# Kernel tuning notes

Measured on AMD Instinct MI355X. Metric: run time of the kernel, lower is better.

The kernel has to match this reference:

```python
import jax, jax.numpy as jnp
import numpy as np

# CUBA-LIF constants (from LavaNetwork.__init__ with beta=0.95)
THRESHOLD = 1.0
CURRENT_DECAY = 1.0   # current[t] = (1-1.0)*current[t-1] + input[t] == input[t]
VOLTAGE_DECAY = 1.0 - 0.95  # = 0.05, so v[t] = 0.95*v[t-1] + cur[t]

N_INPUT, N_HIDDEN, N_OUTPUT = 512, 2048, 4 * 64
B, T = 32, 1024


def setup_inputs() -> dict:
    key = jax.random.key(0)
    kx, k1, k2, k3, k4 = jax.random.split(key, 5)
    x = (jax.random.uniform(kx, (B, N_INPUT, T)) < 0.1).astype(jnp.float32)
    # learned params (Linear with bias); small scale so spiking is reasonable
    w1 = jax.random.normal(k1, (N_HIDDEN, N_INPUT), dtype=jnp.float32) * (1.0 / np.sqrt(N_INPUT))
    b1 = jax.random.normal(k2, (N_HIDDEN,), dtype=jnp.float32) * 0.01
    w2 = jax.random.normal(k3, (N_OUTPUT, N_HIDDEN), dtype=jnp.float32) * (1.0 / np.sqrt(N_HIDDEN))
    b2 = jax.random.normal(k4, (N_OUTPUT,), dtype=jnp.float32) * 0.01
    return {"x": x, "w1": w1, "b1": b1, "w2": w2, "b2": b2}


def _cuba_lif(cur):
    """CUBA neuron with current_decay=1 (current==synaptic input),
    leaky-integrate voltage, fire at threshold, reset voltage to 0.
    cur: (B, N, T) -> spikes (B, N, T)."""
    beta_v = 1.0 - VOLTAGE_DECAY  # 0.95

    def step(v, c_t):
        v = v * beta_v + c_t
        s = (v >= THRESHOLD).astype(v.dtype)
        v = v * (1.0 - s)  # reset-to-zero on spike (Loihi behavior)
        return v, s

    cur_t = jnp.moveaxis(cur, -1, 0)  # (T, B, N)
    v0 = jnp.zeros(cur.shape[:-1], cur.dtype)
    _, spk = jax.lax.scan(step, v0, cur_t)
    return jnp.moveaxis(spk, 0, -1)  # (B, N, T)


def reference(x, w1, b1, w2, b2):
    # layer 1: synapse (einsum 'bit,oi->bot' + bias) -> CUBA neuron
    cur1 = jnp.einsum('bit,oi->bot', x, w1) + b1[None, :, None]
    spk1 = _cuba_lif(cur1)
    # layer 2
    cur2 = jnp.einsum('bit,oi->bot', spk1, w2) + b2[None, :, None]
    spk2 = _cuba_lif(cur2)
    return (spk1, spk2)
```

## Files before the change

### kernel.cpp

```cpp
#include <hip/hip_runtime.h>


typedef int i32x4 __attribute__((ext_vector_type(4)));
typedef _Float16 f16x8 __attribute__((ext_vector_type(8)));
typedef _Float16 f16x4 __attribute__((ext_vector_type(4)));
typedef float f32x4 __attribute__((ext_vector_type(4)));

#define GLDS(g, l) __builtin_amdgcn_global_load_lds( \
    (const __attribute__((address_space(1))) void*)(g), \
    (__attribute__((address_space(3))) void*)(l), 16, 0, 0)

#define INV231 4.656612873077392578125e-10


__global__ __launch_bounds__(256) void prep_w8(const float* __restrict__ A,
                                               signed char* __restrict__ wp,
                                               int M, int K)
{
    long gt = (long)blockIdx.x * 256 + threadIdx.x;
    int kq4 = K >> 2;
    int m = (int)(gt / kq4), kq = (int)(gt % kq4);
    int k0 = kq * 4;
    int kt = k0 >> 6, kin = k0 & 63;
    int cw = ((kin >> 4) ^ (m >> 1)) & 3;
    float4 w = *(const float4*)&A[(long)m * K + k0];
    float wv[4] = {w.x, w.y, w.z, w.w};
    int pack[4] = {0, 0, 0, 0};
#pragma unroll
    for (int e = 0; e < 4; e++) {
        long k64 = (long)rint((double)wv[e] * 2147483648.0);
#pragma unroll
        for (int j = 0; j < 3; j++) {
            long r = ((k64 + 128) & 255) - 128;
            pack[j] |= ((int)r & 255) << (e * 8);
            k64 = (k64 - r) >> 8;
        }
        pack[3] |= ((int)k64 & 255) << (e * 8);
    }
#pragma unroll
    for (int p = 0; p < 4; p++)
        *(int*)&wp[(((long)kt * 4 + p) * M + m) * 64 + cw * 16 + (kin & 15)] = pack[p];
}

__global__ __launch_bounds__(256) void prep_x8(const float* __restrict__ x,
                                               unsigned char* __restrict__ xt)
{
    __shared__ float xs[64][68];
    const int b = blockIdx.z, i0 = blockIdx.y * 64, t0 = blockIdx.x * 64;
    const float* xb = x + ((long)b * 512 + i0) * 1024 + t0;
#pragma unroll
    for (int p = 0; p < 4; p++) {
        int f = threadIdx.x + p * 256;
        int i = f >> 4, t4 = (f & 15) * 4;
        *(float4*)&xs[i][t4] = *(const float4*)&xb[(long)i * 1024 + t4];
    }
    __syncthreads();
    int tt = threadIdx.x >> 2, c = threadIdx.x & 3;
    unsigned char bytes[16];
#pragma unroll
    for (int j = 0; j < 16; j++)
        bytes[j] = (unsigned char)xs[c * 16 + j][tt];
    *(uint4*)&xt[(((long)b * 8 + (i0 >> 6)) * 1024 + t0 + tt) * 64 + c * 16] =
        *(uint4*)bytes;
}

template <bool TRANS, int NITER, int CHUNK>
__global__ __launch_bounds__(256, 2) void gemm_i8(
    const signed char* __restrict__ wp,
    const unsigned char* __restrict__ act,
    const float* __restrict__ bias,
    float* __restrict__ C,
    int M)
{
    constexpr int NCHUNK = NITER / CHUNK;
    __shared__ signed char Ws[CHUNK][4][32][64];

    const int b = blockIdx.y;
    const int m0 = blockIdx.z * 32, t0 = blockIdx.x * 256;
    const int tid = threadIdx.x, lane = tid & 63, wave = tid >> 6;
    const int wt = t0 + wave * 64;
    const int lm = lane & 15, lq = lane >> 4;
    const int fro = ((lq ^ (lm >> 1)) & 3) * 16;
    const int gl_row = lane >> 2, gl_col = (lane & 3) * 16;

    const unsigned char* ab = act + (long)b * NITER * 1024 * 64;

    auto stage = [&](int cc) {
#pragma unroll
        for (int j = 0; j < CHUNK; ++j) {
            const int r = wave + 4 * j;
            const int kt = r >> 2, p = r & 3;
            const long kg = ((long)(cc * CHUNK + kt) * 4 + p);
            const signed char* g = wp + (kg * M + m0 + gl_row) * 64 + gl_col;
            GLDS(g, &Ws[kt][p][0][0]);
            GLDS(g + 16 * 64, &Ws[kt][p][16][0]);
        }
    };

    i32x4 acc[4][8];
#pragma unroll
    for (int p = 0; p < 4; p++)
#pragma unroll
        for (int q = 0; q < 8; q++) acc[p][q] = (i32x4)0;

    stage(0);
    i32x4 areg[2][4];
#pragma unroll
    for (int f = 0; f < 4; f++)
        areg[0][f] = *(const i32x4*)&ab[((long)(wt + f * 16 + lm)) * 64 + lq * 16];
    __syncthreads();

    for (int c = 0; c < NCHUNK; ++c) {
#pragma unroll
        for (int kk = 0; kk < CHUNK; ++kk) {
            {
                const int itv = c * CHUNK + kk;
                const long nx = (itv + 1 < NITER) ? itv + 1 : itv;
#pragma unroll
                for (int f = 0; f < 4; f++)
                    areg[(kk + 1) & 1][f] = *(const i32x4*)
                        &ab[(nx * 1024 + wt + f * 16 + lm) * 64 + lq * 16];
            }
#pragma unroll
            for (int p = 0; p < 4; p++) {
                i32x4 w0 = *(const i32x4*)&Ws[kk][p][lm][fro];
                i32x4 w1 = *(const i32x4*)&Ws[kk][p][16 + lm][fro];
                if (TRANS) {
#pragma unroll
                    for (int f = 0; f < 4; f++) {
                        acc[p][f * 2 + 0] = __builtin_amdgcn_mfma_i32_16x16x64_i8(
                            areg[kk & 1][f], w0, acc[p][f * 2 + 0], 0, 0, 0);
                        acc[p][f * 2 + 1] = __builtin_amdgcn_mfma_i32_16x16x64_i8(
                            areg[kk & 1][f], w1, acc[p][f * 2 + 1], 0, 0, 0);
                    }
                } else {
#pragma unroll
                    for (int f = 0; f < 4; f++) {
                        acc[p][0 + f] = __builtin_amdgcn_mfma_i32_16x16x64_i8(
                            w0, areg[kk & 1][f], acc[p][0 + f], 0, 0, 0);
                        acc[p][4 + f] = __builtin_amdgcn_mfma_i32_16x16x64_i8(
                            w1, areg[kk & 1][f], acc[p][4 + f], 0, 0, 0);
                    }
                }
            }
        }
        if (c + 1 < NCHUNK) {
            __syncthreads();
            stage(c + 1);
            __syncthreads();
        }
    }

    if (TRANS) {
        double bv[2];
        bv[0] = (double)bias[m0 + lm];
        bv[1] = (double)bias[m0 + 16 + lm];
        float* Cb = C + (long)b * 1024 * M;
#pragma unroll
        for (int tf = 0; tf < 4; tf++)
#pragma unroll
            for (int r = 0; r < 4; r++) {
                const int trow = wt + tf * 16 + lq * 4 + r;
#pragma unroll
                for (int mf = 0; mf < 2; mf++) {
                    long T = acc[3][tf * 2 + mf][r];
                    T = T * 256 + acc[2][tf * 2 + mf][r];
                    T = T * 256 + acc[1][tf * 2 + mf][r];
                    T = T * 256 + acc[0][tf * 2 + mf][r];
                    Cb[(long)trow * M + m0 + mf * 16 + lm] =
                        (float)((double)T * INV231 + bv[mf]);
                }
            }
    } else {
        float* Cb = C + (long)b * M * 1024;
#pragma unroll
        for (int mf = 0; mf < 2; mf++)
#pragma unroll
            for (int r = 0; r < 4; r++) {
                const int mrow = m0 + mf * 16 + lq * 4 + r;
                const double bv = (double)bias[mrow];
#pragma unroll
                for (int tf = 0; tf < 4; tf++) {
                    long T = acc[3][mf * 4 + tf][r];
                    T = T * 256 + acc[2][mf * 4 + tf][r];
                    T = T * 256 + acc[1][mf * 4 + tf][r];
                    T = T * 256 + acc[0][mf * 4 + tf][r];
                    Cb[(long)mrow * 1024 + wt + tf * 16 + lm] =
                        (float)((double)T * INV231 + bv);
                }
            }
    }
}


__global__ __launch_bounds__(256) void lif1_t(
    const float* __restrict__ ct,
    unsigned char* __restrict__ spk8,
    unsigned* __restrict__ mask_ws)
{
    const int b = blockIdx.y;
    const int m = blockIdx.x * 256 + threadIdx.x;
    const float* src = ct + (long)b * 1024 * 2048 + m;
    unsigned char* spb = spk8 + (((long)b * 32 + (m >> 6)) * 1024) * 64 + (m & 63);
    unsigned* mw = mask_ws + (long)b * 32 * 2048 + m;
    double v = 0.0;
    float c0[32], c1[32];
#pragma unroll
    for (int j = 0; j < 32; j++)
        c0[j] = src[(long)j * 2048];
    for (int tw = 0; tw < 32; tw += 2) {
#pragma unroll
        for (int j = 0; j < 32; j++)
            c1[j] = src[(long)((tw + 1) * 32 + j) * 2048];
        unsigned mword = 0;
#pragma unroll
        for (int j = 0; j < 32; j++) {
            v = 0.95 * v + (double)c0[j];
            bool s = v >= 1.0;
            mword |= (s ? 1u : 0u) << j;
            if (s) v = 0.0;
            spb[(long)(tw * 32 + j) * 64] = s ? 1 : 0;
        }
        mw[(long)tw * 2048] = mword;
        if (tw + 2 < 32) {
#pragma unroll
            for (int j = 0; j < 32; j++)
                c0[j] = src[(long)((tw + 2) * 32 + j) * 2048];
        }
        mword = 0;
#pragma unroll
        for (int j = 0; j < 32; j++) {
            v = 0.95 * v + (double)c1[j];
            bool s = v >= 1.0;
            mword |= (s ? 1u : 0u) << j;
            if (s) v = 0.0;
            spb[(long)((tw + 1) * 32 + j) * 64] = s ? 1 : 0;
        }
        mw[(long)(tw + 1) * 2048] = mword;
    }
}

__global__ __launch_bounds__(256) void expand_spk(
    const unsigned* __restrict__ mask_ws,
    float* __restrict__ spk1)
{
    __shared__ unsigned msk[8][32];
    const long rowbase = (long)blockIdx.x * 8;
    const int b = (int)(rowbase >> 11), m0 = (int)(rowbase & 2047);
    const int tid = threadIdx.x;
    {
        int w = tid >> 3, r = tid & 7;
        msk[r][w] = mask_ws[((long)b * 32 + w) * 2048 + m0 + r];
    }
    __syncthreads();
    const int r = tid >> 5, l5 = tid & 31;
    float* dst = spk1 + (rowbase + r) * 1024;
    const int sh = (l5 & 7) * 4;
#pragma unroll
    for (int j = 0; j < 8; j++) {
        const int t = l5 * 4 + j * 128;
        const unsigned w = msk[r][(l5 >> 3) + j * 4];
        float4 o;
        o.x = ((w >> sh) & 1u) ? 1.f : 0.f;
        o.y = ((w >> (sh + 1)) & 1u) ? 1.f : 0.f;
        o.z = ((w >> (sh + 2)) & 1u) ? 1.f : 0.f;
        o.w = ((w >> (sh + 3)) & 1u) ? 1.f : 0.f;
        *(float4*)&dst[t] = o;
    }
}

template <int RPB>
__global__ __launch_bounds__(256) void lif_lds(float* __restrict__ cur)
{
    __shared__ float cs[RPB][36];
    const long rowbase = (long)blockIdx.x * RPB;
    float* base = cur + rowbase * 1024;
    const int tid = threadIdx.x;
    double v = 0.0;
    const int NV = RPB * 32 / 4;
    for (int tc = 0; tc < 1024; tc += 32) {
        for (int f = tid; f < NV; f += 256) {
            int row = f >> 3, t4 = (f & 7) * 4;
            *(float4*)&cs[row][t4] = *(const float4*)&base[(long)row * 1024 + tc + t4];
        }
        __syncthreads();
        if (tid < RPB) {
#pragma unroll
            for (int j = 0; j < 32; j++) {
                v = 0.95 * v + (double)cs[tid][j];
                bool s = v >= 1.0;
                cs[tid][j] = s ? 1.f : 0.f;
                if (s) v = 0.0;
            }
        }
        __syncthreads();
        for (int f = tid; f < NV; f += 256) {
            int row = f >> 3, t4 = (f & 7) * 4;
            *(float4*)&base[(long)row * 1024 + tc + t4] = *(float4*)&cs[row][t4];
        }
        __syncthreads();
    }
}


__device__ inline void split3(float w, _Float16& q0, _Float16& q1, _Float16& q2) {
    float p0 = rintf(w * 4096.f) * 2.44140625e-4f;
    float r1 = w - p0;
    float p1s = rintf(r1 * 8388608.f) * 2.44140625e-4f;
    float r2 = r1 - p1s * 4.8828125e-4f;
    float p2s = rintf(r2 * 1.7179869184e10f) * 1.220703125e-4f;
    q0 = (_Float16)p0; q1 = (_Float16)p1s; q2 = (_Float16)p2s;
}

__global__ __launch_bounds__(256) void gemm_f16x3_kernel(
    const float* __restrict__ A, const float* __restrict__ Bmat,
    const float* __restrict__ bias, float* __restrict__ C,
    int M, int N, int K, long sB, long sC)
{
    __shared__ _Float16 As[3][128][40];
    __shared__ _Float16 Bsh[128][40];
    const int batch = blockIdx.z;
    const float* Bp = Bmat + (long)batch * sB;
    float* Cp = C + (long)batch * sC;
    const int m0 = blockIdx.y * 128, n0 = blockIdx.x * 128;
    const int tid = threadIdx.x, lane = tid & 63, wave = tid >> 6;
    const int wrow = (wave >> 1) * 64, wcol = (wave & 1) * 64;
    const int lm = lane & 15, lq = lane >> 4;
    const int a_mo = tid >> 3, a_kc = (tid & 7) * 4;
    const int b_kq = tid >> 5, b_nq = tid & 31;

    f32x4 acc[3][4][4];
#pragma unroll
    for (int p = 0; p < 3; p++)
#pragma unroll
        for (int i = 0; i < 4; i++)
#pragma unroll
            for (int j = 0; j < 4; j++) acc[p][i][j] = (f32x4)0.f;

    for (int k0 = 0; k0 < K; k0 += 32) {
#pragma unroll
        for (int i = 0; i < 4; i++) {
            const int m = i * 32 + a_mo;
            float4 w = *(const float4*)&A[(long)(m0 + m) * K + k0 + a_kc];
            _Float16 a0[4], a1[4], a2[4];
            split3(w.x, a0[0], a1[0], a2[0]);
            split3(w.y, a0[1], a1[1], a2[1]);
            split3(w.z, a0[2], a1[2], a2[2]);
            split3(w.w, a0[3], a1[3], a2[3]);
            *(f16x4*)&As[0][m][a_kc] = (f16x4){a0[0], a0[1], a0[2], a0[3]};
            *(f16x4*)&As[1][m][a_kc] = (f16x4){a1[0], a1[1], a1[2], a1[3]};
            *(f16x4*)&As[2][m][a_kc] = (f16x4){a2[0], a2[1], a2[2], a2[3]};
        }
        {
            float4 r0 = *(const float4*)&Bp[(long)(k0 + b_kq * 4 + 0) * N + n0 + b_nq * 4];
            float4 r1 = *(const float4*)&Bp[(long)(k0 + b_kq * 4 + 1) * N + n0 + b_nq * 4];
            float4 r2 = *(const float4*)&Bp[(long)(k0 + b_kq * 4 + 2) * N + n0 + b_nq * 4];
            float4 r3 = *(const float4*)&Bp[(long)(k0 + b_kq * 4 + 3) * N + n0 + b_nq * 4];
            *(f16x4*)&Bsh[b_nq * 4 + 0][b_kq * 4] =
                (f16x4){(_Float16)r0.x, (_Float16)r1.x, (_Float16)r2.x, (_Float16)r3.x};
            *(f16x4*)&Bsh[b_nq * 4 + 1][b_kq * 4] =
                (f16x4){(_Float16)r0.y, (_Float16)r1.y, (_Float16)r2.y, (_Float16)r3.y};
            *(f16x4*)&Bsh[b_nq * 4 + 2][b_kq * 4] =
                (f16x4){(_Float16)r0.z, (_Float16)r1.z, (_Float16)r2.z, (_Float16)r3.z};
            *(f16x4*)&Bsh[b_nq * 4 + 3][b_kq * 4] =
                (f16x4){(_Float16)r0.w, (_Float16)r1.w, (_Float16)r2.w, (_Float16)r3.w};
        }
        __syncthreads();
        f16x8 bf[4];
#pragma unroll
        for (int j = 0; j < 4; j++)
            bf[j] = *(const f16x8*)&Bsh[wcol + j * 16 + lm][lq * 8];
#pragma unroll
        for (int p = 0; p < 3; p++) {
            f16x8 af[4];
#pragma unroll
            for (int i = 0; i < 4; i++)
                af[i] = *(const f16x8*)&As[p][wrow + i * 16 + lm][lq * 8];
#pragma unroll
            for (int i = 0; i < 4; i++)
#pragma unroll
                for (int j = 0; j < 4; j++)
                    acc[p][i][j] = __builtin_amdgcn_mfma_f32_16x16x32_f16(
                        af[i], bf[j], acc[p][i][j], 0, 0, 0);
        }
        __syncthreads();
    }
#pragma unroll
    for (int i = 0; i < 4; i++)
#pragma unroll
        for (int r = 0; r < 4; r++) {
            const int row = m0 + wrow + i * 16 + lq * 4 + r;
            const double bv = (double)bias[row];
#pragma unroll
            for (int j = 0; j < 4; j++) {
                double s = (double)acc[0][i][j][r]
                         + (double)acc[1][i][j][r] * 4.8828125e-4
                         + (double)acc[2][i][j][r] * 4.76837158203125e-7 + bv;
                Cp[(long)row * N + n0 + wcol + j * 16 + lm] = (float)s;
            }
        }
}

__global__ __launch_bounds__(256) void lif_rows(float* __restrict__ data,
                                                long nrows, int T)
{
    long r = (long)blockIdx.x * blockDim.x + threadIdx.x;
    if (r >= nrows) return;
    float* p = data + r * (long)T;
    double v = 0.0;
    for (int t = 0; t < T; t += 4) {
        float4 c = *(float4*)(p + t);
        float4 s;
        v = 0.95 * v + (double)c.x; s.x = (v >= 1.0) ? 1.f : 0.f; if (v >= 1.0) v = 0.0;
        v = 0.95 * v + (double)c.y; s.y = (v >= 1.0) ? 1.f : 0.f; if (v >= 1.0) v = 0.0;
        v = 0.95 * v + (double)c.z; s.z = (v >= 1.0) ? 1.f : 0.f; if (v >= 1.0) v = 0.0;
        v = 0.95 * v + (double)c.w; s.w = (v >= 1.0) ? 1.f : 0.f; if (v >= 1.0) v = 0.0;
        *(float4*)(p + t) = s;
    }
}


extern "C" void kernel_launch(void* const* d_in, const int* in_sizes, int n_in,
                              void* d_out, int out_size, void* d_ws, size_t ws_size,
                              hipStream_t stream)
{
    const float* x  = (const float*)d_in[0];
    const float* w1 = (const float*)d_in[1];
    const float* b1 = (const float*)d_in[2];
    const float* w2 = (const float*)d_in[3];
    const float* b2 = (const float*)d_in[4];

    float* out  = (float*)d_out;
    float* spk1 = out;
    float* spk2 = out + (long)32 * 2048 * 1024;

    const size_t WP1 = 4194304;
    const size_t WP2 = 2097152;
    const size_t X8T = 16777216;
    const size_t SPK = 67108864;
    const size_t MSK = 8388608;
    const size_t NEED = WP1 + WP2 + X8T + SPK + MSK;

    if (ws_size >= NEED) {
        char* ws = (char*)d_ws;
        signed char* wp1 = (signed char*)ws;
        signed char* wp2 = (signed char*)(ws + WP1);
        unsigned char* x8t = (unsigned char*)(ws + WP1 + WP2);
        unsigned char* spk8 = (unsigned char*)(ws + WP1 + WP2 + X8T);
        unsigned* mask_ws = (unsigned*)(ws + WP1 + WP2 + X8T + SPK);

        prep_w8<<<1024, 256, 0, stream>>>(w1, wp1, 2048, 512);
        prep_w8<<<512, 256, 0, stream>>>(w2, wp2, 256, 2048);
        prep_x8<<<dim3(16, 8, 32), 256, 0, stream>>>(x, x8t);

        gemm_i8<true, 8, 8><<<dim3(4, 32, 64), 256, 0, stream>>>(
            wp1, x8t, b1, spk1, 2048);
        lif1_t<<<dim3(8, 32), 256, 0, stream>>>(spk1, spk8, mask_ws);
        expand_spk<<<8192, 256, 0, stream>>>(mask_ws, spk1);

        gemm_i8<false, 32, 8><<<dim3(4, 32, 8), 256, 0, stream>>>(
            wp2, spk8, b2, spk2, 256);
        lif_lds<32><<<256, 256, 0, stream>>>(spk2);
    } else {
        gemm_f16x3_kernel<<<dim3(8, 16, 32), 256, 0, stream>>>(
            w1, x, b1, spk1, 2048, 1024, 512, (long)512 * 1024, (long)2048 * 1024);
        lif_rows<<<(65536 + 255) / 256, 256, 0, stream>>>(spk1, 65536, 1024);
        gemm_f16x3_kernel<<<dim3(8, 2, 32), 256, 0, stream>>>(
            w2, spk1, b2, spk2, 256, 1024, 2048, (long)2048 * 1024, (long)256 * 1024);
        lif_rows<<<(8192 + 255) / 256, 256, 0, stream>>>(spk2, 8192, 1024);
    }
}
```

Baseline: 684.1 us.

## Fuse layer-1 int8 GEMM with LIF scan via extra LIF wave

Replaces the separate layer-1 GEMM, which wrote a full fp32 current tensor, and the LIF kernel with one fused kernel. Four MFMA waves compute 256-timestep current tiles into a double-buffered LDS array while a fifth wave runs the sequential LIF scan on the previous tile and writes spike bitmasks. A new kernel expands the bitmasks into the int8 activation layout for layer 2. This removes the round trip of the large fp32 layer-1 current tensor through global memory. In exchange the scan is serialized inside each block with only 32 lanes of one wave active, and per-block occupancy drops because of the larger LDS footprint.

```diff
diff --git a/kernel.cpp b/kernel.cpp
--- a/kernel.cpp
+++ b/kernel.cpp
@@ -64,179 +64,146 @@
         *(uint4*)bytes;
 }
 
-template <bool TRANS, int NITER, int CHUNK>
-__global__ __launch_bounds__(256, 2) void gemm_i8(
+__global__ __launch_bounds__(320) void gemm_lif1(
     const signed char* __restrict__ wp,
     const unsigned char* __restrict__ act,
     const float* __restrict__ bias,
-    float* __restrict__ C,
-    int M)
-{
-    constexpr int NCHUNK = NITER / CHUNK;
-    __shared__ signed char Ws[CHUNK][4][32][64];
-
-    const int b = blockIdx.y;
-    const int m0 = blockIdx.z * 32, t0 = blockIdx.x * 256;
+    unsigned* __restrict__ mask_ws)
+{
+    __shared__ signed char Ws[8][4][32][64];
+    __shared__ float cs[2][256][33];
+
+    const int b = blockIdx.x, m0 = blockIdx.y * 32;
     const int tid = threadIdx.x, lane = tid & 63, wave = tid >> 6;
-    const int wt = t0 + wave * 64;
     const int lm = lane & 15, lq = lane >> 4;
     const int fro = ((lq ^ (lm >> 1)) & 3) * 16;
-    const int gl_row = lane >> 2, gl_col = (lane & 3) * 16;
-
-    const unsigned char* ab = act + (long)b * NITER * 1024 * 64;
-
-    auto stage = [&](int cc) {
-#pragma unroll
-        for (int j = 0; j < CHUNK; ++j) {
+    const unsigned char* ab = act + (long)b * 8 * 1024 * 64;
+
+    i32x4 areg[2][4];
+    double bv0 = 0.0, bv1 = 0.0;
+
+    if (wave < 4) {
+        const int gl_row = lane >> 2, gl_col = (lane & 3) * 16;
+#pragma unroll
+        for (int j = 0; j < 8; ++j) {
             const int r = wave + 4 * j;
             const int kt = r >> 2, p = r & 3;
-            const long kg = ((long)(cc * CHUNK + kt) * 4 + p);
-            const signed char* g = wp + (kg * M + m0 + gl_row) * 64 + gl_col;
+            const signed char* g = wp + ((long)r * 2048 + m0 + gl_row) * 64 + gl_col;
             GLDS(g, &Ws[kt][p][0][0]);
             GLDS(g + 16 * 64, &Ws[kt][p][16][0]);
         }
-    };
-
-    i32x4 acc[4][8];
-#pragma unroll
-    for (int p = 0; p < 4; p++)
-#pragma unroll
-        for (int q = 0; q < 8; q++) acc[p][q] = (i32x4)0;
-
-    stage(0);
-    i32x4 areg[2][4];
-#pragma unroll
-    for (int f = 0; f < 4; f++)
-        areg[0][f] = *(const i32x4*)&ab[((long)(wt + f * 16 + lm)) * 64 + lq * 16];
+        bv0 = (double)bias[m0 + lm];
+        bv1 = (double)bias[m0 + 16 + lm];
+#pragma unroll
+        for (int f = 0; f < 4; f++)
+            areg[0][f] = *(const i32x4*)
+                &ab[((long)(wave * 64 + f * 16 + lm)) * 64 + lq * 16];
+    }
     __syncthreads();
 
-    for (int c = 0; c < NCHUNK; ++c) {
-#pragma unroll
-        for (int kk = 0; kk < CHUNK; ++kk) {
-            {
-                const int itv = c * CHUNK + kk;
-                const long nx = (itv + 1 < NITER) ? itv + 1 : itv;
-#pragma unroll
-                for (int f = 0; f < 4; f++)
-                    areg[(kk + 1) & 1][f] = *(const i32x4*)
-                        &ab[(nx * 1024 + wt + f * 16 + lm) * 64 + lq * 16];
-            }
-#pragma unroll
-            for (int p = 0; p < 4; p++) {
-                i32x4 w0 = *(const i32x4*)&Ws[kk][p][lm][fro];
-                i32x4 w1 = *(const i32x4*)&Ws[kk][p][16 + lm][fro];
-                if (TRANS) {
+    double u = 0.0;
+    bool sprev = false;
+
+    for (int p = 0; p < 5; ++p) {
+        if (wave < 4 && p < 4) {
+            i32x4 acc[4][8];
+#pragma unroll
+            for (int pp = 0; pp < 4; pp++)
+#pragma unroll
+                for (int q = 0; q < 8; q++) acc[pp][q] = (i32x4)0;
+
+#pragma unroll
+            for (int kk = 0; kk < 8; ++kk) {
+                {
+                    int pn = p, kn = kk + 1;
+                    if (kn == 8) { kn = 0; pn = p + 1; if (pn > 3) { pn = 3; kn = 7; } }
+                    const long tt = (long)pn * 256 + wave * 64 + lm;
+#pragma unroll
+                    for (int f = 0; f < 4; f++)
+                        areg[(kk + 1) & 1][f] = *(const i32x4*)
+                            &ab[((long)kn * 1024 + tt + f * 16) * 64 + lq * 16];
+                }
+#pragma unroll
+                for (int pp = 0; pp < 4; pp++) {
+                    i32x4 w0 = *(const i32x4*)&Ws[kk][pp][lm][fro];
+                    i32x4 w1 = *(const i32x4*)&Ws[kk][pp][16 + lm][fro];
 #pragma unroll
                     for (int f = 0; f < 4; f++) {
-                        acc[p][f * 2 + 0] = __builtin_amdgcn_mfma_i32_16x16x64_i8(
-                            areg[kk & 1][f], w0, acc[p][f * 2 + 0], 0, 0, 0);
-                        acc[p][f * 2 + 1] = __builtin_amdgcn_mfma_i32_16x16x64_i8(
-                            areg[kk & 1][f], w1, acc[p][f * 2 + 1], 0, 0, 0);
+                        acc[pp][f * 2 + 0] = __builtin_amdgcn_mfma_i32_16x16x64_i8(
+                            areg[kk & 1][f], w0, acc[pp][f * 2 + 0], 0, 0, 0);
+                        acc[pp][f * 2 + 1] = __builtin_amdgcn_mfma_i32_16x16x64_i8(
+                            areg[kk & 1][f], w1, acc[pp][f * 2 + 1], 0, 0, 0);
                     }
-                } else {
-#pragma unroll
-                    for (int f = 0; f < 4; f++) {
-                        acc[p][0 + f] = __builtin_amdgcn_mfma_i32_16x16x64_i8(
-                            w0, areg[kk & 1][f], acc[p][0 + f], 0, 0, 0);
-                        acc[p][4 + f] = __builtin_amdgcn_mfma_i32_16x16x64_i8(
-                            w1, areg[kk & 1][f], acc[p][4 + f], 0, 0, 0);
+                }
+            }
+            const int tb = wave * 64;
+#pragma unroll
+            for (int tf = 0; tf < 4; tf++)
+#pragma unroll
+                for (int r = 0; r < 4; r++) {
+                    const int tl = tb + tf * 16 + lq * 4 + r;
+#pragma unroll
+                    for (int mf = 0; mf < 2; mf++) {
+                        long T = acc[3][tf * 2 + mf][r];
+                        T = T * 256 + acc[2][tf * 2 + mf][r];
+                        T = T * 256 + acc[1][tf * 2 + mf][r];
+                        T = T * 256 + acc[0][tf * 2 + mf][r];
+                        cs[p & 1][tl][mf * 16 + lm] =
+                            (float)((double)T * INV231 + (mf ? bv1 : bv0));
                     }
                 }
-            }
-        }
-        if (c + 1 < NCHUNK) {
-            __syncthreads();
-            stage(c + 1);
-            __syncthreads();
-        }
-    }
-
-    if (TRANS) {
-        double bv[2];
-        bv[0] = (double)bias[m0 + lm];
-        bv[1] = (double)bias[m0 + 16 + lm];
-        float* Cb = C + (long)b * 1024 * M;
-#pragma unroll
-        for (int tf = 0; tf < 4; tf++)
-#pragma unroll
-            for (int r = 0; r < 4; r++) {
-                const int trow = wt + tf * 16 + lq * 4 + r;
-#pragma unroll
-                for (int mf = 0; mf < 2; mf++) {
-                    long T = acc[3][tf * 2 + mf][r];
-                    T = T * 256 + acc[2][tf * 2 + mf][r];
-                    T = T * 256 + acc[1][tf * 2 + mf][r];
-                    T = T * 256 + acc[0][tf * 2 + mf][r];
-                    Cb[(long)trow * M + m0 + mf * 16 + lm] =
-                        (float)((double)T * INV231 + bv[mf]);
-                }
-            }
-    } else {
-        float* Cb = C + (long)b * M * 1024;
-#pragma unroll
-        for (int mf = 0; mf < 2; mf++)
-#pragma unroll
-            for (int r = 0; r < 4; r++) {
-                const int mrow = m0 + mf * 16 + lq * 4 + r;
-                const double bv = (double)bias[mrow];
-#pragma unroll
-                for (int tf = 0; tf < 4; tf++) {
-                    long T = acc[3][mf * 4 + tf][r];
-                    T = T * 256 + acc[2][mf * 4 + tf][r];
-                    T = T * 256 + acc[1][mf * 4 + tf][r];
-                    T = T * 256 + acc[0][mf * 4 + tf][r];
-                    Cb[(long)mrow * 1024 + wt + tf * 16 + lm] =
-                        (float)((double)T * INV231 + bv);
-                }
-            }
-    }
-}
-
-
-__global__ __launch_bounds__(256) void lif1_t(
-    const float* __restrict__ ct,
-    unsigned char* __restrict__ spk8,
-    unsigned* __restrict__ mask_ws)
-{
-    const int b = blockIdx.y;
-    const int m = blockIdx.x * 256 + threadIdx.x;
-    const float* src = ct + (long)b * 1024 * 2048 + m;
-    unsigned char* spb = spk8 + (((long)b * 32 + (m >> 6)) * 1024) * 64 + (m & 63);
-    unsigned* mw = mask_ws + (long)b * 32 * 2048 + m;
-    double v = 0.0;
-    float c0[32], c1[32];
-#pragma unroll
-    for (int j = 0; j < 32; j++)
-        c0[j] = src[(long)j * 2048];
-    for (int tw = 0; tw < 32; tw += 2) {
-#pragma unroll
-        for (int j = 0; j < 32; j++)
-            c1[j] = src[(long)((tw + 1) * 32 + j) * 2048];
-        unsigned mword = 0;
-#pragma unroll
-        for (int j = 0; j < 32; j++) {
-            v = 0.95 * v + (double)c0[j];
-            bool s = v >= 1.0;
-            mword |= (s ? 1u : 0u) << j;
-            if (s) v = 0.0;
-            spb[(long)(tw * 32 + j) * 64] = s ? 1 : 0;
-        }
-        mw[(long)tw * 2048] = mword;
-        if (tw + 2 < 32) {
-#pragma unroll
-            for (int j = 0; j < 32; j++)
-                c0[j] = src[(long)((tw + 2) * 32 + j) * 2048];
-        }
-        mword = 0;
-#pragma unroll
-        for (int j = 0; j < 32; j++) {
-            v = 0.95 * v + (double)c1[j];
-            bool s = v >= 1.0;
-            mword |= (s ? 1u : 0u) << j;
-            if (s) v = 0.0;
-            spb[(long)((tw + 1) * 32 + j) * 64] = s ? 1 : 0;
-        }
-        mw[(long)(tw + 1) * 2048] = mword;
+        }
+        if (wave == 4 && p >= 1 && lane < 32) {
+            const int pp = p - 1, buf = pp & 1;
+#pragma unroll 1
+            for (int g = 0; g < 8; ++g) {
+                unsigned mword = 0;
+#pragma unroll
+                for (int j = 0; j < 32; ++j) {
+                    double c = (double)cs[buf][g * 32 + j][lane];
+                    double a = 0.95 * u + c;
+                    u = sprev ? c : a;
+                    bool s = (u >= 1.0);
+                    mword |= (s ? 1u : 0u) << j;
+                    sprev = s;
+                }
+                mask_ws[((long)b * 32 + pp * 8 + g) * 2048 + m0 + lane] = mword;
+            }
+        }
+        __syncthreads();
+    }
+}
+
+
+__global__ __launch_bounds__(256) void expand_spk8(
+    const unsigned* __restrict__ mask_ws,
+    unsigned char* __restrict__ spk8)
+{
+    __shared__ unsigned msk[64][33];
+    const int b = blockIdx.x, kt = blockIdx.y;
+    const int tid = threadIdx.x;
+#pragma unroll
+    for (int i = 0; i < 8; ++i) {
+        int idx = tid + i * 256;
+        int tw = idx >> 6, m = idx & 63;
+        msk[m][tw] = mask_ws[((long)b * 32 + tw) * 2048 + kt * 64 + m];
+    }
+    __syncthreads();
+    unsigned char* dst = spk8 + ((long)b * 32 + kt) * 1024 * 64;
+#pragma unroll
+    for (int i = 0; i < 16; ++i) {
+        int off = tid + i * 256;
+        int t = off >> 2, mq = off & 3;
+        int tw = t >> 5, sh = t & 31;
+        unsigned w0 = 0, w1 = 0, w2 = 0, w3 = 0;
+#pragma unroll
+        for (int j = 0; j < 4; ++j) {
+            w0 |= ((msk[mq * 16 + j][tw] >> sh) & 1u) << (8 * j);
+            w1 |= ((msk[mq * 16 + 4 + j][tw] >> sh) & 1u) << (8 * j);
+            w2 |= ((msk[mq * 16 + 8 + j][tw] >> sh) & 1u) << (8 * j);
+            w3 |= ((msk[mq * 16 + 12 + j][tw] >> sh) & 1u) << (8 * j);
+        }
+        *(uint4*)&dst[(long)off * 16] = (uint4){w0, w1, w2, w3};
     }
 }
 
@@ -266,6 +233,134 @@
         o.z = ((w >> (sh + 2)) & 1u) ? 1.f : 0.f;
         o.w = ((w >> (sh + 3)) & 1u) ? 1.f : 0.f;
         *(float4*)&dst[t] = o;
+    }
+}
+
+template <bool TRANS, int NITER, int CHUNK>
+__global__ __launch_bounds__(256, 2) void gemm_i8(
+    const signed char* __restrict__ wp,
+    const unsigned char* __restrict__ act,
+    const float* __restrict__ bias,
+    float* __restrict__ C,
+    int M)
+{
+    constexpr int NCHUNK = NITER / CHUNK;
+    __shared__ signed char Ws[CHUNK][4][32][64];
+
+    const int b = blockIdx.y;
+    const int m0 = blockIdx.z * 32, t0 = blockIdx.x * 256;
+    const int tid = threadIdx.x, lane = tid & 63, wave = tid >> 6;
+    const int wt = t0 + wave * 64;
+    const int lm = lane & 15, lq = lane >> 4;
+    const int fro = ((lq ^ (lm >> 1)) & 3) * 16;
+    const int gl_row = lane >> 2, gl_col = (lane & 3) * 16;
+
+    const unsigned char* ab = act + (long)b * NITER * 1024 * 64;
+
+    auto stage = [&](int cc) {
+#pragma unroll
+        for (int j = 0; j < CHUNK; ++j) {
+            const int r = wave + 4 * j;
+            const int kt = r >> 2, p = r & 3;
+            const long kg = ((long)(cc * CHUNK + kt) * 4 + p);
+            const signed char* g = wp + (kg * M + m0 + gl_row) * 64 + gl_col;
+            GLDS(g, &Ws[kt][p][0][0]);
+            GLDS(g + 16 * 64, &Ws[kt][p][16][0]);
+        }
+    };
+
+    i32x4 acc[4][8];
+#pragma unroll
+    for (int p = 0; p < 4; p++)
+#pragma unroll
+        for (int q = 0; q < 8; q++) acc[p][q] = (i32x4)0;
+
+    stage(0);
+    i32x4 areg[2][4];
+#pragma unroll
+    for (int f = 0; f < 4; f++)
+        areg[0][f] = *(const i32x4*)&ab[((long)(wt + f * 16 + lm)) * 64 + lq * 16];
+    __syncthreads();
+
+    for (int c = 0; c < NCHUNK; ++c) {
+#pragma unroll
+        for (int kk = 0; kk < CHUNK; ++kk) {
+            {
+                const int itv = c * CHUNK + kk;
+                const long nx = (itv + 1 < NITER) ? itv + 1 : itv;
+#pragma unroll
+                for (int f = 0; f < 4; f++)
+                    areg[(kk + 1) & 1][f] = *(const i32x4*)
+                        &ab[(nx * 1024 + wt + f * 16 + lm) * 64 + lq * 16];
+            }
+#pragma unroll
+            for (int p = 0; p < 4; p++) {
+                i32x4 w0 = *(const i32x4*)&Ws[kk][p][lm][fro];
+                i32x4 w1 = *(const i32x4*)&Ws[kk][p][16 + lm][fro];
+                if (TRANS) {
+#pragma unroll
+                    for (int f = 0; f < 4; f++) {
+                        acc[p][f * 2 + 0] = __builtin_amdgcn_mfma_i32_16x16x64_i8(
+                            areg[kk & 1][f], w0, acc[p][f * 2 + 0], 0, 0, 0);
+                        acc[p][f * 2 + 1] = __builtin_amdgcn_mfma_i32_16x16x64_i8(
+                            areg[kk & 1][f], w1, acc[p][f * 2 + 1], 0, 0, 0);
+                    }
+                } else {
+#pragma unroll
+                    for (int f = 0; f < 4; f++) {
+                        acc[p][0 + f] = __builtin_amdgcn_mfma_i32_16x16x64_i8(
+                            w0, areg[kk & 1][f], acc[p][0 + f], 0, 0, 0);
+                        acc[p][4 + f] = __builtin_amdgcn_mfma_i32_16x16x64_i8(
+                            w1, areg[kk & 1][f], acc[p][4 + f], 0, 0, 0);
+                    }
+                }
+            }
+        }
+        if (c + 1 < NCHUNK) {
+            __syncthreads();
+            stage(c + 1);
+            __syncthreads();
+        }
+    }
+
+    if (TRANS) {
+        double bv[2];
+        bv[0] = (double)bias[m0 + lm];
+        bv[1] = (double)bias[m0 + 16 + lm];
+        float* Cb = C + (long)b * 1024 * M;
+#pragma unroll
+        for (int tf = 0; tf < 4; tf++)
+#pragma unroll
+            for (int r = 0; r < 4; r++) {
+                const int trow = wt + tf * 16 + lq * 4 + r;
+#pragma unroll
+                for (int mf = 0; mf < 2; mf++) {
+                    long T = acc[3][tf * 2 + mf][r];
+                    T = T * 256 + acc[2][tf * 2 + mf][r];
+                    T = T * 256 + acc[1][tf * 2 + mf][r];
+                    T = T * 256 + acc[0][tf * 2 + mf][r];
+                    Cb[(long)trow * M + m0 + mf * 16 + lm] =
+                        (float)((double)T * INV231 + bv[mf]);
+                }
+            }
+    } else {
+        float* Cb = C + (long)b * M * 1024;
+#pragma unroll
+        for (int mf = 0; mf < 2; mf++)
+#pragma unroll
+            for (int r = 0; r < 4; r++) {
+                const int mrow = m0 + mf * 16 + lq * 4 + r;
+                const double bv = (double)bias[mrow];
+#pragma unroll
+                for (int tf = 0; tf < 4; tf++) {
+                    long T = acc[3][mf * 4 + tf][r];
+                    T = T * 256 + acc[2][mf * 4 + tf][r];
+                    T = T * 256 + acc[1][mf * 4 + tf][r];
+                    T = T * 256 + acc[0][mf * 4 + tf][r];
+                    Cb[(long)mrow * 1024 + wt + tf * 16 + lm] =
+                        (float)((double)T * INV231 + bv);
+                }
+            }
     }
 }
 
@@ -453,14 +548,14 @@
         prep_w8<<<512, 256, 0, stream>>>(w2, wp2, 256, 2048);
         prep_x8<<<dim3(16, 8, 32), 256, 0, stream>>>(x, x8t);
 
-        gemm_i8<true, 8, 8><<<dim3(4, 32, 64), 256, 0, stream>>>(
-            wp1, x8t, b1, spk1, 2048);
-        lif1_t<<<dim3(8, 32), 256, 0, stream>>>(spk1, spk8, mask_ws);
-        expand_spk<<<8192, 256, 0, stream>>>(mask_ws, spk1);
+        gemm_lif1<<<dim3(32, 64), 320, 0, stream>>>(wp1, x8t, b1, mask_ws);
+        expand_spk8<<<dim3(32, 32), 256, 0, stream>>>(mask_ws, spk8);
 
         gemm_i8<false, 32, 8><<<dim3(4, 32, 8), 256, 0, stream>>>(
             wp2, spk8, b2, spk2, 256);
         lif_lds<32><<<256, 256, 0, stream>>>(spk2);
+
+        expand_spk<<<8192, 256, 0, stream>>>(mask_ws, spk1);
     } else {
         gemm_f16x3_kernel<<<dim3(8, 16, 32), 256, 0, stream>>>(
             w1, x, b1, spk1, 2048, 1024, 512, (long)512 * 1024, (long)2048 * 1024);
```

After: 677.4 us. About the same (-1.0%).
